# Optimization experiments

Measured on AMD Instinct MI355X. Metric: run time of the kernel, lower is better.

The kernel has to match this reference:

```python
import jax, jax.numpy as jnp
import numpy as np

DIM = 2048
H = 16
HKV = 4
D = DIM // H          # 128 head_dim
ROPE_BASE = 10000.0
TRAIN_SEQ_LEN = 1024
EPS = float(np.finfo(np.float32).eps)  # torch F.rms_norm default eps


def setup_inputs() -> dict:
    key = jax.random.key(0)
    ks = jax.random.split(key, 6)
    B, T = 2, 2048
    return {
        "x": jax.random.normal(ks[0], (B, T, DIM), jnp.float32),
        "q_w": jax.random.normal(ks[1], (DIM, DIM), jnp.float32) * 0.02,
        "k_w": jax.random.normal(ks[2], (HKV * D, DIM), jnp.float32) * 0.02,
        "v_w": jax.random.normal(ks[3], (HKV * D, DIM), jnp.float32) * 0.02,
        "out_w": jax.random.normal(ks[4], (DIM, DIM), jnp.float32) * 0.02,
        "q_gain": jnp.ones((H,), jnp.float32),
    }


def _rope_tables(T, dtype):
    rd = D  # rope_dims == head_dim (rope_dims=0 in module)
    if T > TRAIN_SEQ_LEN:
        scale = T / TRAIN_SEQ_LEN
        base = ROPE_BASE * scale ** (rd / (rd - 2))
    else:
        base = ROPE_BASE
    inv_freq = 1.0 / base ** (np.arange(0, rd, 2, dtype=np.float32) / rd)
    t = np.arange(T, dtype=np.float32)
    freqs = np.outer(t, inv_freq)  # [T, rd/2]
    cos = jnp.asarray(np.cos(freqs), dtype)[None, :, None, :]  # [1,T,1,rd/2]
    sin = jnp.asarray(np.sin(freqs), dtype)[None, :, None, :]
    return cos, sin


def _rms_norm(x):
    var = jnp.mean(jnp.square(x), axis=-1, keepdims=True)
    return x * jax.lax.rsqrt(var + EPS)


def _apply_rotary(x, cos, sin):
    half = x.shape[-1] // 2
    x1, x2 = x[..., :half], x[..., half:]
    return jnp.concatenate((x1 * cos + x2 * sin, -x1 * sin + x2 * cos), axis=-1)


def reference(x, q_w, k_w, v_w, out_w, q_gain):
    B, T, dim = x.shape
    q = (x @ q_w.T).reshape(B, T, H, D)
    k = (x @ k_w.T).reshape(B, T, HKV, D)
    v = (x @ v_w.T).reshape(B, T, HKV, D)
    q = _rms_norm(q)
    k = _rms_norm(k)
    cos, sin = _rope_tables(T, q.dtype)
    q = _apply_rotary(q, cos, sin)
    k = _apply_rotary(k, cos, sin)
    q = q * q_gain[None, None, :, None]
    rep = H // HKV
    k_r = jnp.repeat(k, rep, axis=2)  # [B,T,H,D]
    v_r = jnp.repeat(v, rep, axis=2)
    scores = jnp.einsum('bqhd,bkhd->bhqk', q, k_r) / jnp.sqrt(jnp.asarray(D, q.dtype))
    causal = jnp.tril(jnp.ones((T, T), bool))
    scores = jnp.where(causal[None, None], scores, jnp.asarray(-jnp.inf, scores.dtype))
    p = jax.nn.softmax(scores, axis=-1)
    y = jnp.einsum('bhqk,bkhd->bqhd', p, v_r).reshape(B, T, dim)
    return y @ out_w.T
```

## Files before the change

### kernel.cpp

```cpp
#include <hip/hip_runtime.h>
#include <hip/hip_bf16.h>

typedef __bf16 bf16x8 __attribute__((ext_vector_type(8)));
typedef unsigned short u16x8 __attribute__((ext_vector_type(8)));
typedef float f32x4 __attribute__((ext_vector_type(4)));
typedef __hip_bfloat16 bf16;

#define GLOAD_LDS16(g, l)                                               \
  __builtin_amdgcn_global_load_lds(                                     \
      (__attribute__((address_space(1))) void*)(void*)(g),              \
      (__attribute__((address_space(3))) void*)(void*)(l), 16, 0, 0)

__global__ __launch_bounds__(256) void cvt_all(
    const float4* __restrict__ x,  const float4* __restrict__ qw,
    const float4* __restrict__ kw, const float4* __restrict__ vw,
    const float4* __restrict__ ow,
    ushort4* __restrict__ xb,  ushort4* __restrict__ qwb,
    ushort4* __restrict__ kwb, ushort4* __restrict__ vwb,
    ushort4* __restrict__ owb)
{
  const int i = blockIdx.x * 256 + threadIdx.x;
  const float4* s; ushort4* d; int off;
  if      (i < 2097152) { s = x;  d = xb;  off = i; }
  else if (i < 3145728) { s = qw; d = qwb; off = i - 2097152; }
  else if (i < 3407872) { s = kw; d = kwb; off = i - 3145728; }
  else if (i < 3670016) { s = vw; d = vwb; off = i - 3407872; }
  else                  { s = ow; d = owb; off = i - 3670016; }
  float4 v = s[off];
  bf16 b0 = __float2bfloat16(v.x), b1 = __float2bfloat16(v.y);
  bf16 b2 = __float2bfloat16(v.z), b3 = __float2bfloat16(v.w);
  ushort4 o;
  o.x = *(unsigned short*)&b0; o.y = *(unsigned short*)&b1;
  o.z = *(unsigned short*)&b2; o.w = *(unsigned short*)&b3;
  d[off] = o;
}

__device__ __forceinline__ void store_out(bf16* p, float v)  { *p = __float2bfloat16(v); }
__device__ __forceinline__ void store_out(float* p, float v) { *p = v; }

template <typename OutT, int K>
__device__ __forceinline__ void gemm256_body(
    const bf16* __restrict__ Ag, const bf16* __restrict__ Wg, OutT* __restrict__ C,
    int bm, int bn, int N, bf16* As0, bf16* As1, bf16* Bs0, bf16* Bs1)
{
  constexpr int NT = K / 64;
  const int tid   = threadIdx.x;
  const int lane  = tid & 63;
  const int w     = tid >> 6;
  const int wr    = w >> 2;
  const int wc    = w & 3;
  const int mfrag = lane & 15;
  const int quad  = lane >> 4;
  const int m7x16 = (mfrag & 7) << 4;

  auto stage_half = [&](const bf16* __restrict__ G, int grow0, int k0, bf16* dsthalf) {
#pragma unroll
    for (int l = 0; l < 2; ++l) {
      const int o    = l * 8192 + tid * 16;
      const int row  = o >> 7;
      const int slot = ((o >> 4) & 7) ^ (row & 7);
      const bf16* src = G + (size_t)(grow0 + row) * K + k0 + slot * 8;
      GLOAD_LDS16(src, (char*)dsthalf + l * 8192 + w * 1024);
    }
  };

  stage_half(Ag, bm,       0, As0);
  stage_half(Ag, bm + 128, 0, As0 + 8192);
  stage_half(Wg, bn,       0, Bs0);
  stage_half(Wg, bn + 128, 0, Bs0 + 8192);
  if (NT > 1) {
    stage_half(Wg, bn,       64, Bs1);
    stage_half(Wg, bn + 128, 64, Bs1 + 8192);
    asm volatile("s_waitcnt vmcnt(4)" ::: "memory");
  } else {
    asm volatile("s_waitcnt vmcnt(0)" ::: "memory");
  }
  __builtin_amdgcn_s_barrier();

  f32x4 acc[8][4] = {};

  for (int t = 0; t < NT; ++t) {
    const char* Ab = (const char*)((t & 1) ? As1 : As0);
    const char* Bb = (const char*)((t & 1) ? Bs1 : Bs0);
    bf16* Asn  = (t & 1) ? As0 : As1;
    bf16* Bsn2 = (t & 1) ? Bs1 : Bs0;

    bf16x8 bfr[4][2];
#pragma unroll
    for (int ph = 0; ph < 4; ++ph) {
      if (ph == 0) {
#pragma unroll
        for (int j = 0; j < 4; ++j) {
          const int rn = wc * 64 + j * 16 + mfrag;
#pragma unroll
          for (int kh = 0; kh < 2; ++kh)
            bfr[j][kh] = *(const bf16x8*)(Bb + ((rn * 128 + kh * 64 + quad * 16) ^ m7x16));
        }
      }
      bf16x8 afr[2][2];
#pragma unroll
      for (int r = 0; r < 2; ++r) {
        const int ra = wr * 128 + (ph * 2 + r) * 16 + mfrag;
#pragma unroll
        for (int kh = 0; kh < 2; ++kh)
          afr[r][kh] = *(const bf16x8*)(Ab + ((ra * 128 + kh * 64 + quad * 16) ^ m7x16));
      }

      if (ph == 0 && t + 1 < NT) stage_half(Ag, bm,       (t + 1) * 64, Asn);
      if (ph == 1 && t + 1 < NT) stage_half(Ag, bm + 128, (t + 1) * 64, Asn + 8192);
      if (ph == 2 && t + 2 < NT) stage_half(Wg, bn,       (t + 2) * 64, Bsn2);
      if (ph == 3 && t + 2 < NT) stage_half(Wg, bn + 128, (t + 2) * 64, Bsn2 + 8192);

      __builtin_amdgcn_s_barrier();
      asm volatile("s_waitcnt lgkmcnt(0)" ::: "memory");
      __builtin_amdgcn_s_setprio(1);
#pragma unroll
      for (int r = 0; r < 2; ++r)
#pragma unroll
        for (int j = 0; j < 4; ++j)
#pragma unroll
          for (int kh = 0; kh < 2; ++kh)
            acc[ph * 2 + r][j] = __builtin_amdgcn_mfma_f32_16x16x32_bf16(
                afr[r][kh], bfr[j][kh], acc[ph * 2 + r][j], 0, 0, 0);
      __builtin_amdgcn_s_setprio(0);
      if (ph == 3) {
        if (t < NT - 2) asm volatile("s_waitcnt vmcnt(4)" ::: "memory");
        else            asm volatile("s_waitcnt vmcnt(0)" ::: "memory");
      }
      __builtin_amdgcn_s_barrier();
    }
  }

  const int rq = quad * 4;
#pragma unroll
  for (int i = 0; i < 8; ++i)
#pragma unroll
    for (int j = 0; j < 4; ++j)
#pragma unroll
      for (int r = 0; r < 4; ++r) {
        const int row = bm + wr * 128 + i * 16 + rq + r;
        const int col = bn + wc * 64 + j * 16 + mfrag;
        store_out(&C[(size_t)row * N + col], acc[i][j][r]);
      }
}

__global__ __launch_bounds__(512, 2) void gemm_qkv256(
    const bf16* __restrict__ X,  const bf16* __restrict__ Wq,
    const bf16* __restrict__ Wk, const bf16* __restrict__ Wv,
    bf16* __restrict__ Qo, bf16* __restrict__ Ko, bf16* __restrict__ Vo)
{
  __shared__ alignas(16) bf16 As[2][16384];
  __shared__ alignas(16) bf16 Bs[2][16384];
  const int bx = blockIdx.x;
  const bf16* W; bf16* C; int N, bn;
  if (bx < 8)       { W = Wq; C = Qo; N = 2048; bn = bx * 256; }
  else if (bx < 10) { W = Wk; C = Ko; N = 512;  bn = (bx - 8) * 256; }
  else              { W = Wv; C = Vo; N = 512;  bn = (bx - 10) * 256; }
  gemm256_body<bf16, 2048>(X, W, C, blockIdx.y * 256, bn, N,
                           As[0], As[1], Bs[0], Bs[1]);
}

__global__ __launch_bounds__(512, 2) void gemm_out256(
    const bf16* __restrict__ A, const bf16* __restrict__ W, float* __restrict__ C)
{
  __shared__ alignas(16) bf16 As[2][16384];
  __shared__ alignas(16) bf16 Bs[2][16384];
  gemm256_body<float, 2048>(A, W, C, blockIdx.y * 256, blockIdx.x * 256, 2048,
                            As[0], As[1], Bs[0], Bs[1]);
}

__device__ __forceinline__ void rope_row(
    bf16* __restrict__ buf, const float* __restrict__ gain,
    int nh, float scale, int row)
{
  const int j = threadIdx.x & 63;
  const int bt = row / nh;
  const int h  = row - bt * nh;
  const int t  = bt & 2047;
  bf16* p = buf + (size_t)bt * (nh * 128) + h * 128;

  float x1 = __bfloat162float(p[j]);
  float x2 = __bfloat162float(p[j + 64]);
  float ss = x1 * x1 + x2 * x2;
#pragma unroll
  for (int off = 32; off > 0; off >>= 1) ss += __shfl_xor(ss, off, 64);
  const float rinv = rsqrtf(ss * (1.0f / 128.0f) + 1.1920928955078125e-07f);
  const float g = gain ? gain[h] : 1.0f;
  const float s = rinv * g * scale;

  const float inv_freq = exp2f(-(float)j * (14.3035853954f / 64.0f));
  const float fr = (float)t * inv_freq;
  const float cs = cosf(fr), sn = sinf(fr);
  p[j]      = __float2bfloat16(s * (x1 * cs + x2 * sn));
  p[j + 64] = __float2bfloat16(s * (x2 * cs - x1 * sn));
}

__global__ __launch_bounds__(256) void postqkv(
    bf16* __restrict__ qb, bf16* __restrict__ kb,
    const unsigned short* __restrict__ vb, unsigned short* __restrict__ vtb,
    const float* __restrict__ gain)
{
  const int bx = blockIdx.x;
  if (bx < 16384) {
    rope_row(qb, gain, 16, 0.08838834764831845f, bx * 4 + (threadIdx.x >> 6));
  } else if (bx < 20480) {
    rope_row(kb, nullptr, 4, 1.0f, (bx - 16384) * 4 + (threadIdx.x >> 6));
  } else {
    const int idx = (bx - 20480) * 256 + threadIdx.x;
    const int t  = idx & 4095;
    const int dc = idx >> 12;
    u16x8 v = *(const u16x8*)(vb + (size_t)t * 512 + dc * 8);
#pragma unroll
    for (int j = 0; j < 8; ++j)
      vtb[(size_t)(dc * 8 + j) * 4096 + t] = v[j];
  }
}

__global__ __launch_bounds__(256) void flash_attn(
    const bf16* __restrict__ Q, const bf16* __restrict__ Kg,
    const bf16* __restrict__ Vtg, bf16* __restrict__ Y)
{
  __shared__ bf16 Ks[2][64 * 128];
  __shared__ bf16 Vs[2][128 * 64];
  __shared__ bf16 Ps[4][16 * 64];

  const int tid = threadIdx.x, lane = tid & 63, w = tid >> 6;
  const int p = blockIdx.x & 15, bh = blockIdx.x >> 4;
  const int h = bh & 15, b = bh >> 4, kvh = h >> 2;
  const int mfrag = lane & 15, quad = lane >> 4;
  const int m7 = mfrag & 7;

  auto stage_k = [&](int kt, int s) {
#pragma unroll
    for (int g = 0; g < 4; ++g) {
      const int o = g * 4096 + w * 1024 + lane * 16;
      const int r = o >> 8, c = (o >> 4) & 15;
      const int cs = (c & 8) | ((c ^ (r & 7)) & 7);
      const bf16* src = Kg + ((size_t)(b * 2048 + kt * 64 + r)) * 512 + kvh * 128 + cs * 8;
      GLOAD_LDS16(src, (char*)&Ks[s][0] + g * 4096 + w * 1024);
    }
  };
  auto stage_v = [&](int kt, int s) {
#pragma unroll
    for (int g = 0; g < 4; ++g) {
      const int o = g * 4096 + w * 1024 + lane * 16;
      const int r = o >> 7, c = (o >> 4) & 7;
      const int cs = (c ^ (r & 7)) & 7;
      const bf16* src = Vtg + ((size_t)(kvh * 128 + r)) * 4096 + b * 2048 + kt * 64 + cs * 8;
      GLOAD_LDS16(src, (char*)&Vs[s][0] + g * 4096 + w * 1024);
    }
  };

  stage_k(0, 0);
  stage_v(0, 0);
  int sb = 0;
  bf16* psw = &Ps[w][0];

  for (int phase = 0; phase < 2; ++phase) {
    const int qt = phase ? p : 31 - p;

    bf16x8 qf[4];
    const bf16* qrow = Q + ((size_t)(b * 2048 + qt * 64 + w * 16 + mfrag)) * 2048 + h * 128;
#pragma unroll
    for (int c = 0; c < 4; ++c) qf[c] = *(const bf16x8*)(qrow + c * 32 + quad * 8);

    f32x4 oacc[8] = {};
    float l_lane[4] = {0.f, 0.f, 0.f, 0.f};
    const int q_base = qt * 64 + w * 16 + quad * 4;

    for (int kt = 0; kt <= qt; ++kt) {
      __syncthreads();
      const bool last = (phase == 1) && (kt == qt);
      if (!last) {
        const int nk = kt < qt ? kt + 1 : 0;
        stage_k(nk, sb ^ 1);
        stage_v(nk, sb ^ 1);
      }

      f32x4 sc[4] = {};
#pragma unroll
      for (int kc = 0; kc < 4; ++kc) {
        const bf16* krow = &Ks[sb][0] + (kc * 16 + mfrag) * 128;
#pragma unroll
        for (int c = 0; c < 4; ++c) {
          const int G = 4 * c + quad;
          const int cs = (G & 8) | ((G ^ m7) & 7);
          bf16x8 kf = *(const bf16x8*)(krow + cs * 8);
          sc[kc] = __builtin_amdgcn_mfma_f32_16x16x32_bf16(qf[c], kf, sc[kc], 0, 0, 0);
        }
      }

      if (kt == qt) {
        const int kcol0 = kt * 64 + mfrag;
#pragma unroll
        for (int kc = 0; kc < 4; ++kc)
#pragma unroll
          for (int r = 0; r < 4; ++r)
            if (kcol0 + kc * 16 > q_base + r) sc[kc][r] = -1e30f;
      }

#pragma unroll
      for (int kc = 0; kc < 4; ++kc)
#pragma unroll
        for (int r = 0; r < 4; ++r) {
          const float pv = __expf(sc[kc][r] - 14.0f);
          l_lane[r] += pv;
          const int q = quad * 4 + r;
          const int slot = ((2 * kc + (mfrag >> 3)) ^ (q & 7)) & 7;
          psw[q * 64 + slot * 8 + m7] = __float2bfloat16(pv);
        }

#pragma unroll
      for (int kh = 0; kh < 2; ++kh) {
        const int Gp = 4 * kh + quad;
        const int sl = (Gp ^ m7) & 7;
        bf16x8 pf = *(const bf16x8*)(psw + mfrag * 64 + sl * 8);
#pragma unroll
        for (int dc = 0; dc < 8; ++dc) {
          bf16x8 vf = *(const bf16x8*)(&Vs[sb][0] + (dc * 16 + mfrag) * 64 + sl * 8);
          oacc[dc] = __builtin_amdgcn_mfma_f32_16x16x32_bf16(pf, vf, oacc[dc], 0, 0, 0);
        }
      }
      sb ^= 1;
    }

#pragma unroll
    for (int r = 0; r < 4; ++r) {
      float l = l_lane[r];
      l += __shfl_xor(l, 1, 64);
      l += __shfl_xor(l, 2, 64);
      l += __shfl_xor(l, 4, 64);
      l += __shfl_xor(l, 8, 64);
      const float linv = 1.0f / l;
      const size_t row = (size_t)(b * 2048 + q_base + r);
#pragma unroll
      for (int dc = 0; dc < 8; ++dc)
        Y[row * 2048 + h * 128 + dc * 16 + mfrag] = __float2bfloat16(oacc[dc][r] * linv);
    }
  }
}

extern "C" void kernel_launch(void* const* d_in, const int* in_sizes, int n_in,
                              void* d_out, int out_size, void* d_ws, size_t ws_size,
                              hipStream_t stream)
{
  const float* x      = (const float*)d_in[0];
  const float* q_w    = (const float*)d_in[1];
  const float* k_w    = (const float*)d_in[2];
  const float* v_w    = (const float*)d_in[3];
  const float* o_w    = (const float*)d_in[4];
  const float* q_gain = (const float*)d_in[5];
  float* out = (float*)d_out;

  char* ws = (char*)d_ws;
  bf16* xb  = (bf16*)(ws);
  bf16* yb  = (bf16*)(ws);
  bf16* qwb = (bf16*)(ws + (16u << 20));
  bf16* vtb = (bf16*)(ws + (16u << 20));
  bf16* owb = (bf16*)(ws + (24u << 20));
  bf16* kwb = (bf16*)(ws + (32u << 20));
  bf16* vwb = (bf16*)(ws + (34u << 20));
  bf16* qb  = (bf16*)(ws + (36u << 20));
  bf16* kb  = (bf16*)(ws + (52u << 20));
  bf16* vb  = (bf16*)(ws + (56u << 20));

  cvt_all<<<dim3(18432), dim3(256), 0, stream>>>(
      (const float4*)x, (const float4*)q_w, (const float4*)k_w,
      (const float4*)v_w, (const float4*)o_w,
      (ushort4*)xb, (ushort4*)qwb, (ushort4*)kwb, (ushort4*)vwb, (ushort4*)owb);

  gemm_qkv256<<<dim3(12, 16), dim3(512), 0, stream>>>(xb, qwb, kwb, vwb, qb, kb, vb);

  postqkv<<<dim3(21504), dim3(256), 0, stream>>>(
      qb, kb, (const unsigned short*)vb, (unsigned short*)vtb, q_gain);

  flash_attn<<<dim3(512), dim3(256), 0, stream>>>(qb, kb, vtb, yb);

  gemm_out256<<<dim3(8, 16), dim3(512), 0, stream>>>(yb, owb, out);
}
```

Measured before the change: 315.5 us.

## Use 256x128 tiles for output GEMM, swizzle block order, add MFMA priority hints

Adds a 256x128 GEMM body so the output projection launches 256 blocks instead of 128, filling more compute units. The GEMM kernels also remap block indices to group tiles that share data, aiming for better L2 reuse. s_setprio raises wave priority around the MFMA sections in both the GEMM and the flash attention loops. The narrower tile lowers arithmetic intensity per block and reloads the A operand more often.

New measurement: 312.8 us. Within noise of the previous version (-0.9%).

```diff
diff --git a/kernel.cpp b/kernel.cpp
--- a/kernel.cpp
+++ b/kernel.cpp
@@ -38,12 +38,12 @@
 __device__ __forceinline__ void store_out(bf16* p, float v)  { *p = __float2bfloat16(v); }
 __device__ __forceinline__ void store_out(float* p, float v) { *p = v; }
 
-template <typename OutT, int K>
+template <typename OutT, int LD, int KLEN>
 __device__ __forceinline__ void gemm256_body(
     const bf16* __restrict__ Ag, const bf16* __restrict__ Wg, OutT* __restrict__ C,
     int bm, int bn, int N, bf16* As0, bf16* As1, bf16* Bs0, bf16* Bs1)
 {
-  constexpr int NT = K / 64;
+  constexpr int NT = KLEN / 64;
   const int tid   = threadIdx.x;
   const int lane  = tid & 63;
   const int w     = tid >> 6;
@@ -59,7 +59,7 @@
       const int o    = l * 8192 + tid * 16;
       const int row  = o >> 7;
       const int slot = ((o >> 4) & 7) ^ (row & 7);
-      const bf16* src = G + (size_t)(grow0 + row) * K + k0 + slot * 8;
+      const bf16* src = G + (size_t)(grow0 + row) * LD + k0 + slot * 8;
       GLOAD_LDS16(src, (char*)dsthalf + l * 8192 + w * 1024);
     }
   };
@@ -144,6 +144,105 @@
       }
 }
 
+template <typename OutT, int LD, int KLEN>
+__device__ __forceinline__ void gemm256x128_body(
+    const bf16* __restrict__ Ag, const bf16* __restrict__ Wg, OutT* __restrict__ C,
+    int bm, int bn, int N, bf16* As0, bf16* As1, bf16* Bs0, bf16* Bs1)
+{
+  constexpr int NT = KLEN / 64;
+  const int tid   = threadIdx.x;
+  const int lane  = tid & 63;
+  const int w     = tid >> 6;
+  const int wr    = w >> 2;
+  const int wc    = w & 3;
+  const int mfrag = lane & 15;
+  const int quad  = lane >> 4;
+  const int m7x16 = (mfrag & 7) << 4;
+
+  auto stage_half = [&](const bf16* __restrict__ G, int grow0, int k0, bf16* dsthalf) {
+#pragma unroll
+    for (int l = 0; l < 2; ++l) {
+      const int o    = l * 8192 + tid * 16;
+      const int row  = o >> 7;
+      const int slot = ((o >> 4) & 7) ^ (row & 7);
+      const bf16* src = G + (size_t)(grow0 + row) * LD + k0 + slot * 8;
+      GLOAD_LDS16(src, (char*)dsthalf + l * 8192 + w * 1024);
+    }
+  };
+
+  stage_half(Ag, bm,       0, As0);
+  stage_half(Ag, bm + 128, 0, As0 + 8192);
+  stage_half(Wg, bn, 0, Bs0);
+  stage_half(Wg, bn, 64, Bs1);
+  asm volatile("s_waitcnt vmcnt(2)" ::: "memory");
+  __builtin_amdgcn_s_barrier();
+
+  f32x4 acc[8][2] = {};
+
+  for (int t = 0; t < NT; ++t) {
+    const char* Ab = (const char*)((t & 1) ? As1 : As0);
+    const char* Bb = (const char*)((t & 1) ? Bs1 : Bs0);
+    bf16* Asn  = (t & 1) ? As0 : As1;
+    bf16* Bsn2 = (t & 1) ? Bs1 : Bs0;
+
+    bf16x8 bfr[2][2];
+#pragma unroll
+    for (int ph = 0; ph < 4; ++ph) {
+      if (ph == 0) {
+#pragma unroll
+        for (int j = 0; j < 2; ++j) {
+          const int rn = wc * 32 + j * 16 + mfrag;
+#pragma unroll
+          for (int kh = 0; kh < 2; ++kh)
+            bfr[j][kh] = *(const bf16x8*)(Bb + ((rn * 128 + kh * 64 + quad * 16) ^ m7x16));
+        }
+      }
+      bf16x8 afr[2][2];
+#pragma unroll
+      for (int r = 0; r < 2; ++r) {
+        const int ra = wr * 128 + (ph * 2 + r) * 16 + mfrag;
+#pragma unroll
+        for (int kh = 0; kh < 2; ++kh)
+          afr[r][kh] = *(const bf16x8*)(Ab + ((ra * 128 + kh * 64 + quad * 16) ^ m7x16));
+      }
+
+      if (ph == 0 && t + 1 < NT) stage_half(Ag, bm,       (t + 1) * 64, Asn);
+      if (ph == 1 && t + 1 < NT) stage_half(Ag, bm + 128, (t + 1) * 64, Asn + 8192);
+      if (ph == 2 && t + 2 < NT) stage_half(Wg, bn,       (t + 2) * 64, Bsn2);
+
+      __builtin_amdgcn_s_barrier();
+      asm volatile("s_waitcnt lgkmcnt(0)" ::: "memory");
+      __builtin_amdgcn_s_setprio(1);
+#pragma unroll
+      for (int r = 0; r < 2; ++r)
+#pragma unroll
+        for (int j = 0; j < 2; ++j)
+#pragma unroll
+          for (int kh = 0; kh < 2; ++kh)
+            acc[ph * 2 + r][j] = __builtin_amdgcn_mfma_f32_16x16x32_bf16(
+                afr[r][kh], bfr[j][kh], acc[ph * 2 + r][j], 0, 0, 0);
+      __builtin_amdgcn_s_setprio(0);
+      if (ph == 3) {
+        if (t < NT - 2) asm volatile("s_waitcnt vmcnt(2)" ::: "memory");
+        else            asm volatile("s_waitcnt vmcnt(0)" ::: "memory");
+      }
+      __builtin_amdgcn_s_barrier();
+    }
+  }
+
+  const int rq = quad * 4;
+#pragma unroll
+  for (int i = 0; i < 8; ++i)
+#pragma unroll
+    for (int j = 0; j < 2; ++j)
+#pragma unroll
+      for (int r = 0; r < 4; ++r) {
+        const int row = bm + wr * 128 + i * 16 + rq + r;
+        const int col = bn + wc * 32 + j * 16 + mfrag;
+        store_out(&C[(size_t)row * N + col], acc[i][j][r]);
+      }
+}
+
 __global__ __launch_bounds__(512, 2) void gemm_qkv256(
     const bf16* __restrict__ X,  const bf16* __restrict__ Wq,
     const bf16* __restrict__ Wk, const bf16* __restrict__ Wv,
@@ -151,22 +250,29 @@
 {
   __shared__ alignas(16) bf16 As[2][16384];
   __shared__ alignas(16) bf16 Bs[2][16384];
-  const int bx = blockIdx.x;
+  const int orig = blockIdx.y * 12 + blockIdx.x;
+  const int swz  = (orig & 7) * 24 + (orig >> 3);
+  const int bx   = swz % 12;
+  const int by   = swz / 12;
   const bf16* W; bf16* C; int N, bn;
   if (bx < 8)       { W = Wq; C = Qo; N = 2048; bn = bx * 256; }
   else if (bx < 10) { W = Wk; C = Ko; N = 512;  bn = (bx - 8) * 256; }
   else              { W = Wv; C = Vo; N = 512;  bn = (bx - 10) * 256; }
-  gemm256_body<bf16, 2048>(X, W, C, blockIdx.y * 256, bn, N,
-                           As[0], As[1], Bs[0], Bs[1]);
+  gemm256_body<bf16, 2048, 2048>(X, W, C, by * 256, bn, N,
+                                 As[0], As[1], Bs[0], Bs[1]);
 }
 
 __global__ __launch_bounds__(512, 2) void gemm_out256(
     const bf16* __restrict__ A, const bf16* __restrict__ W, float* __restrict__ C)
 {
   __shared__ alignas(16) bf16 As[2][16384];
-  __shared__ alignas(16) bf16 Bs[2][16384];
-  gemm256_body<float, 2048>(A, W, C, blockIdx.y * 256, blockIdx.x * 256, 2048,
-                            As[0], As[1], Bs[0], Bs[1]);
+  __shared__ alignas(16) bf16 Bs[2][8192];
+  const int orig = blockIdx.y * 16 + blockIdx.x;
+  const int swz  = (orig & 7) * 32 + (orig >> 3);
+  const int bx   = swz & 15;
+  const int by   = swz >> 4;
+  gemm256x128_body<float, 2048, 2048>(A, W, C, by * 256, bx * 128, 2048,
+                                      As[0], As[1], Bs[0], Bs[1]);
 }
 
 __device__ __forceinline__ void rope_row(
@@ -278,6 +384,7 @@
       }
 
       f32x4 sc[4] = {};
+      __builtin_amdgcn_s_setprio(1);
 #pragma unroll
       for (int kc = 0; kc < 4; ++kc) {
         const bf16* krow = &Ks[sb][0] + (kc * 16 + mfrag) * 128;
@@ -289,6 +396,7 @@
           sc[kc] = __builtin_amdgcn_mfma_f32_16x16x32_bf16(qf[c], kf, sc[kc], 0, 0, 0);
         }
       }
+      __builtin_amdgcn_s_setprio(0);
 
       if (kt == qt) {
         const int kcol0 = kt * 64 + mfrag;
@@ -310,6 +418,7 @@
           psw[q * 64 + slot * 8 + m7] = __float2bfloat16(pv);
         }
 
+      __builtin_amdgcn_s_setprio(1);
 #pragma unroll
       for (int kh = 0; kh < 2; ++kh) {
         const int Gp = 4 * kh + quad;
@@ -321,6 +430,7 @@
           oacc[dc] = __builtin_amdgcn_mfma_f32_16x16x32_bf16(pf, vf, oacc[dc], 0, 0, 0);
         }
       }
+      __builtin_amdgcn_s_setprio(0);
       sb ^= 1;
     }
 
@@ -376,5 +486,5 @@
 
   flash_attn<<<dim3(512), dim3(256), 0, stream>>>(qb, kb, vtb, yb);
 
-  gemm_out256<<<dim3(8, 16), dim3(512), 0, stream>>>(yb, owb, out);
-}
+  gemm_out256<<<dim3(16, 16), dim3(512), 0, stream>>>(yb, owb, out);
+}
```
